# Kernel optimization log

Hardware: AMD Instinct MI355X
Metric: run time of the kernel (lower is better)

Reference implementation:

```python
import jax, jax.numpy as jnp
import numpy as np

B, L, DM, H = 2, 4096, 1024, 16
D = DM // H


def setup_inputs() -> dict:
    key = jax.random.key(0)
    ks = jax.random.split(key, 11)
    s = 1.0 / np.sqrt(DM)
    return {
        "query": jax.random.normal(ks[0], (B, L, DM), jnp.float32),
        "key": jax.random.normal(ks[1], (B, L, DM), jnp.float32),
        "value": jax.random.normal(ks[2], (B, L, DM), jnp.float32),
        "Wq": jax.random.normal(ks[3], (DM, DM), jnp.float32) * s,
        "bq": jnp.zeros((DM,), jnp.float32),
        "Wk": jax.random.normal(ks[4], (DM, DM), jnp.float32) * s,
        "bk": jnp.zeros((DM,), jnp.float32),
        "Wv": jax.random.normal(ks[5], (DM, DM), jnp.float32) * s,
        "bv": jnp.zeros((DM,), jnp.float32),
        "Wo": jax.random.normal(ks[6], (DM, DM), jnp.float32) * s,
        "bo": jnp.zeros((DM,), jnp.float32),
    }


def _split_heads(x):
    # (B, L, DM) -> (B, H, L, D)
    b, l, _ = x.shape
    return x.reshape(b, l, H, D).transpose(0, 2, 1, 3)


def reference(query, key, value, Wq, bq, Wk, bk, Wv, bv, Wo, bo):
    q = _split_heads(query @ Wq + bq)
    k = _split_heads(key @ Wk + bk)
    v = _split_heads(value @ Wv + bv)
    # ELU+1 feature map
    q = jax.nn.elu(q) + 1.0
    k = jax.nn.elu(k) + 1.0
    # Original: kv = einsum('bhld,bhmd->bhlm', k, v); out = einsum('bhlm,bhld->bhmd', kv, q)
    # Equivalent (associativity): out[m,d] = sum_e v[m,e] * (sum_l k[l,e] q[l,d])
    S = jnp.einsum('bhle,bhld->bhed', k, q)          # (B,H,D,D)
    out = jnp.einsum('bhme,bhed->bhmd', v, S)        # (B,H,L,D)
    denom = jnp.einsum('bhld,bhld->bhl', q, k) + 1e-6
    out = out / denom[..., None]
    # combine heads: (B,H,L,D) -> (B,L,DM)
    out = out.transpose(0, 2, 1, 3).reshape(out.shape[0], -1, DM)
    # out_dense; dropout is identity at inference
    return out @ Wo + bo
```

## Files before the change

### kernel.cpp

```cpp
#include <hip/hip_runtime.h>

#define B_  2
#define L_  4096
#define DM_ 1024
#define H_  16
#define D_  64
#define M_  (B_ * L_)

typedef unsigned short u16;
typedef short bf16x8 __attribute__((ext_vector_type(8)));
typedef float f32x4  __attribute__((ext_vector_type(4)));

typedef const __attribute__((address_space(1))) void* as1_cvp;
typedef __attribute__((address_space(3))) void* as3_vp;

__device__ __forceinline__ float b2f(u16 u) {
    union { unsigned int i; float f; } x; x.i = ((unsigned int)u) << 16; return x.f;
}
__device__ __forceinline__ u16 f2b(float f) {
    unsigned int x = __float_as_uint(f);
    return (u16)((x + 0x7fffu + ((x >> 16) & 1u)) >> 16);
}

__global__ void cast3_bf16_kernel(const float* __restrict__ i0, const float* __restrict__ i1,
                                  const float* __restrict__ i2,
                                  u16* __restrict__ o0, u16* __restrict__ o1, u16* __restrict__ o2,
                                  int n4) {
    int z = blockIdx.z;
    const float* in = z == 0 ? i0 : (z == 1 ? i1 : i2);
    u16* out       = z == 0 ? o0 : (z == 1 ? o1 : o2);
    int i = blockIdx.x * blockDim.x + threadIdx.x;
    if (i < n4) {
        float4 v = ((const float4*)in)[i];
        ushort4 o;
        o.x = f2b(v.x); o.y = f2b(v.y); o.z = f2b(v.z); o.w = f2b(v.w);
        ((ushort4*)out)[i] = o;
    }
}

__global__ void transpose4_cast_kernel(const float* __restrict__ w0, const float* __restrict__ w1,
                                       const float* __restrict__ w2, const float* __restrict__ w3,
                                       u16* __restrict__ t0, u16* __restrict__ t1,
                                       u16* __restrict__ t2, u16* __restrict__ t3) {
    int z = blockIdx.z;
    const float* W = z == 0 ? w0 : z == 1 ? w1 : z == 2 ? w2 : w3;
    u16* Wt        = z == 0 ? t0 : z == 1 ? t1 : z == 2 ? t2 : t3;
    __shared__ float tile[32][33];
    int tx = threadIdx.x, ty = threadIdx.y;
    int n = blockIdx.x * 32 + tx;
    int k0 = blockIdx.y * 32;
#pragma unroll
    for (int i = 0; i < 4; ++i)
        tile[ty + i * 8][tx] = W[(size_t)(k0 + ty + i * 8) * DM_ + n];
    __syncthreads();
#pragma unroll
    for (int i = 0; i < 4; ++i) {
        int nn = blockIdx.x * 32 + ty + i * 8;
        Wt[(size_t)nn * DM_ + k0 + tx] = f2b(tile[tx][ty + i * 8]);
    }
}

__global__ void zero_f32_kernel(float* __restrict__ p, int n) {
    int i = blockIdx.x * blockDim.x + threadIdx.x;
    if (i < n) p[i] = 0.f;
}

__global__ __launch_bounds__(256, 3) void gemm_qkv_kernel(
    const u16* __restrict__ qb, const u16* __restrict__ kb, const u16* __restrict__ vb,
    const u16* __restrict__ Wqt, const u16* __restrict__ Wkt, const u16* __restrict__ Wvt,
    const float* __restrict__ bq, const float* __restrict__ bk, const float* __restrict__ bv,
    u16* __restrict__ QpT, u16* __restrict__ KpT, u16* __restrict__ Vp)
{
    const int z = blockIdx.z;
    const u16* A    = z == 0 ? qb  : z == 1 ? kb  : vb;
    const u16* Bt   = z == 0 ? Wqt : z == 1 ? Wkt : Wvt;
    const float* bias = z == 0 ? bq : z == 1 ? bk : bv;

    __shared__ __align__(16) u16 smem[17408];
    u16* As = smem;
    u16* Bs = smem + 8192;

    const int t    = threadIdx.x;
    const int lane = t & 63;
    const int wave = t >> 6;
    const int wr   = wave >> 1;
    const int wc   = wave & 1;
    const int quad = lane >> 4;
    const int l16  = lane & 15;
    const int m0   = blockIdx.x * 128;
    const int n0   = blockIdx.y * 128;
    const int K    = DM_;

    f32x4 acc[4][4] = {};

    for (int kt = 0; kt < K; kt += 64) {
#pragma unroll
        for (int i = 0; i < 4; ++i) {
            int c   = i * 256 + t;
            int row = c >> 3;
            int kc  = c & 7;
            int cbase = i * 256 + wave * 64;
            const u16* gA = A  + (size_t)(m0 + row) * K + kt + kc * 8;
            const u16* gB = Bt + (size_t)(n0 + row) * K + kt + kc * 8;
            __builtin_amdgcn_global_load_lds((as1_cvp)gA, (as3_vp)(As + cbase * 8), 16, 0, 0);
            __builtin_amdgcn_global_load_lds((as1_cvp)gB, (as3_vp)(Bs + cbase * 8), 16, 0, 0);
        }
        __syncthreads();
#pragma unroll
        for (int ks = 0; ks < 2; ++ks) {
            bf16x8 af[4], bfr[4];
#pragma unroll
            for (int it = 0; it < 4; ++it)
                af[it] = *(const bf16x8*)(As + (wr * 64 + it * 16 + l16) * 64 + ks * 32 + quad * 8);
#pragma unroll
            for (int jt = 0; jt < 4; ++jt)
                bfr[jt] = *(const bf16x8*)(Bs + (wc * 64 + jt * 16 + l16) * 64 + ks * 32 + quad * 8);
#pragma unroll
            for (int it = 0; it < 4; ++it)
#pragma unroll
                for (int jt = 0; jt < 4; ++jt)
                    acc[it][jt] = __builtin_amdgcn_mfma_f32_16x16x32_bf16(
                        af[it], bfr[jt], acc[it][jt], 0, 0, 0);
        }
        __syncthreads();
    }

    if (z == 2) {
#pragma unroll
        for (int it = 0; it < 4; ++it) {
            int row0 = m0 + wr * 64 + it * 16 + quad * 4;
#pragma unroll
            for (int jt = 0; jt < 4; ++jt) {
                int col = n0 + wc * 64 + jt * 16 + l16;
                float bv2 = bias[col];
#pragma unroll
                for (int r = 0; r < 4; ++r)
                    Vp[(size_t)(row0 + r) * DM_ + col] = f2b(acc[it][jt][r] + bv2);
            }
        }
    } else {
        u16* OutT = z == 0 ? QpT : KpT;
        u16* Ct = smem;
#pragma unroll
        for (int it = 0; it < 4; ++it) {
            int row0 = wr * 64 + it * 16 + quad * 4;
#pragma unroll
            for (int jt = 0; jt < 4; ++jt) {
                int colr = wc * 64 + jt * 16 + l16;
                float bv2 = bias[n0 + colr];
                float x0 = acc[it][jt][0] + bv2;
                float x1 = acc[it][jt][1] + bv2;
                float x2 = acc[it][jt][2] + bv2;
                float x3 = acc[it][jt][3] + bv2;
                x0 = (x0 > 0.f) ? (x0 + 1.f) : __expf(x0);
                x1 = (x1 > 0.f) ? (x1 + 1.f) : __expf(x1);
                x2 = (x2 > 0.f) ? (x2 + 1.f) : __expf(x2);
                x3 = (x3 > 0.f) ? (x3 + 1.f) : __expf(x3);
                ushort4 o;
                o.x = f2b(x0); o.y = f2b(x1); o.z = f2b(x2); o.w = f2b(x3);
                *(ushort4*)&Ct[colr * 136 + row0] = o;
            }
        }
        __syncthreads();
        int b   = m0 >> 12;
        int seg = t & 15;
        int cg  = t >> 4;
#pragma unroll
        for (int iter = 0; iter < 8; ++iter) {
            int colIdx = iter * 16 + cg;
            int gcol = n0 + colIdx;
            int bh = b * 16 + (gcol >> 6);
            int e  = gcol & 63;
            uint4 v = *(const uint4*)&Ct[colIdx * 136 + seg * 8];
            *(uint4*)(OutT + ((size_t)bh << 18) + ((size_t)e << 12)
                      + (m0 & 4095) + seg * 8) = v;
        }
    }
}

__global__ __launch_bounds__(256, 3) void gemm_out_kernel(
    const u16* __restrict__ A, const u16* __restrict__ Bt,
    const float* __restrict__ bias, float* __restrict__ Cout)
{
    __shared__ __align__(16) u16 smem[16384];
    u16* As = smem;
    u16* Bs = smem + 8192;

    const int t    = threadIdx.x;
    const int lane = t & 63;
    const int wave = t >> 6;
    const int wr   = wave >> 1;
    const int wc   = wave & 1;
    const int quad = lane >> 4;
    const int l16  = lane & 15;
    const int m0   = blockIdx.x * 128;
    const int n0   = blockIdx.y * 128;
    const int K    = DM_;

    f32x4 acc[4][4] = {};

    for (int kt = 0; kt < K; kt += 64) {
#pragma unroll
        for (int i = 0; i < 4; ++i) {
            int c   = i * 256 + t;
            int row = c >> 3;
            int kc  = c & 7;
            int cbase = i * 256 + wave * 64;
            const u16* gA = A  + (size_t)(m0 + row) * K + kt + kc * 8;
            const u16* gB = Bt + (size_t)(n0 + row) * K + kt + kc * 8;
            __builtin_amdgcn_global_load_lds((as1_cvp)gA, (as3_vp)(As + cbase * 8), 16, 0, 0);
            __builtin_amdgcn_global_load_lds((as1_cvp)gB, (as3_vp)(Bs + cbase * 8), 16, 0, 0);
        }
        __syncthreads();
#pragma unroll
        for (int ks = 0; ks < 2; ++ks) {
            bf16x8 af[4], bfr[4];
#pragma unroll
            for (int it = 0; it < 4; ++it)
                af[it] = *(const bf16x8*)(As + (wr * 64 + it * 16 + l16) * 64 + ks * 32 + quad * 8);
#pragma unroll
            for (int jt = 0; jt < 4; ++jt)
                bfr[jt] = *(const bf16x8*)(Bs + (wc * 64 + jt * 16 + l16) * 64 + ks * 32 + quad * 8);
#pragma unroll
            for (int it = 0; it < 4; ++it)
#pragma unroll
                for (int jt = 0; jt < 4; ++jt)
                    acc[it][jt] = __builtin_amdgcn_mfma_f32_16x16x32_bf16(
                        af[it], bfr[jt], acc[it][jt], 0, 0, 0);
        }
        __syncthreads();
    }

#pragma unroll
    for (int it = 0; it < 4; ++it) {
        int row0 = m0 + wr * 64 + it * 16 + quad * 4;
#pragma unroll
        for (int jt = 0; jt < 4; ++jt) {
            int col = n0 + wc * 64 + jt * 16 + l16;
            float bv = bias[col];
#pragma unroll
            for (int r = 0; r < 4; ++r)
                Cout[(size_t)(row0 + r) * DM_ + col] = acc[it][jt][r] + bv;
        }
    }
}

__global__ __launch_bounds__(256) void attn_s_kernel(
    const u16* __restrict__ QpT, const u16* __restrict__ KpT,
    float* __restrict__ S, float* __restrict__ denom)
{
    const int t    = threadIdx.x;
    const int lane = t & 63;
    const int wave = t >> 6;
    const int quad = lane >> 4;
    const int l16  = lane & 15;
    const int bh   = blockIdx.x;
    const int lc   = blockIdx.y * 512;

    const u16* baseQ = QpT + ((size_t)bh << 18);
    const u16* baseK = KpT + ((size_t)bh << 18);

    f32x4 acc[4] = {};
    const u16* arow = baseK + (size_t)(wave * 16 + l16) * 4096 + lc;
#pragma unroll 4
    for (int ks = 0; ks < 16; ++ks) {
        int koff = ks * 32 + quad * 8;
        bf16x8 a = *(const bf16x8*)(arow + koff);
#pragma unroll
        for (int dt = 0; dt < 4; ++dt) {
            bf16x8 b = *(const bf16x8*)(baseQ + (size_t)(dt * 16 + l16) * 4096 + lc + koff);
            acc[dt] = __builtin_amdgcn_mfma_f32_16x16x32_bf16(a, b, acc[dt], 0, 0, 0);
        }
    }
    float* Sb = S + (size_t)bh * 4096;
#pragma unroll
    for (int dt = 0; dt < 4; ++dt)
#pragma unroll
        for (int r = 0; r < 4; ++r)
            atomicAdd(&Sb[(wave * 16 + quad * 4 + r) * 64 + dt * 16 + l16], acc[dt][r]);

    {
        float s0 = 0.f, s1 = 0.f;
        int off = lc + 2 * t;
#pragma unroll 8
        for (int e = 0; e < 64; ++e) {
            unsigned int qv = *(const unsigned int*)(baseQ + (size_t)e * 4096 + off);
            unsigned int kv = *(const unsigned int*)(baseK + (size_t)e * 4096 + off);
            s0 += b2f((u16)(qv & 0xffff)) * b2f((u16)(kv & 0xffff));
            s1 += b2f((u16)(qv >> 16))   * b2f((u16)(kv >> 16));
        }
        denom[(size_t)bh * 4096 + off]     = s0 + 1e-6f;
        denom[(size_t)bh * 4096 + off + 1] = s1 + 1e-6f;
    }
}

__global__ __launch_bounds__(256) void attn_out_kernel(
    const u16* __restrict__ Vp, const float* __restrict__ S,
    const float* __restrict__ denom, u16* __restrict__ ctx)
{
    __shared__ __align__(16) u16 Sb[64 * 64];
    __shared__ float dsh[256];
    const int t    = threadIdx.x;
    const int lane = t & 63;
    const int wave = t >> 6;
    const int quad = lane >> 4;
    const int l16  = lane & 15;
    const int bh   = blockIdx.x;
    const int b    = bh >> 4, h = bh & 15;
    const int lc   = blockIdx.y * 256;

    {
        const float* Sg = S + (size_t)bh * 4096;
        int e = t >> 2, d0 = (t & 3) * 16;
#pragma unroll
        for (int i = 0; i < 16; ++i)
            Sb[(d0 + i) * 64 + e] = f2b(Sg[e * 64 + d0 + i]);
        dsh[t] = denom[(size_t)bh * 4096 + lc + t];
    }
    __syncthreads();

    const u16* Abase = Vp + (size_t)b * L_ * DM_ + (size_t)(lc + wave * 64 + l16) * DM_ + h * 64;
    f32x4 acc[4][4] = {};
#pragma unroll
    for (int ks = 0; ks < 2; ++ks) {
        int koff = ks * 32 + quad * 8;
        bf16x8 af[4], bfr[4];
#pragma unroll
        for (int lt = 0; lt < 4; ++lt)
            af[lt] = *(const bf16x8*)(Abase + (size_t)(lt * 16) * DM_ + koff);
#pragma unroll
        for (int dt = 0; dt < 4; ++dt)
            bfr[dt] = *(const bf16x8*)(Sb + (dt * 16 + l16) * 64 + koff);
#pragma unroll
        for (int lt = 0; lt < 4; ++lt)
#pragma unroll
            for (int dt = 0; dt < 4; ++dt)
                acc[lt][dt] = __builtin_amdgcn_mfma_f32_16x16x32_bf16(
                    af[lt], bfr[dt], acc[lt][dt], 0, 0, 0);
    }

    u16* cbase = ctx + (size_t)b * L_ * DM_ + h * 64;
#pragma unroll
    for (int lt = 0; lt < 4; ++lt) {
        int lrow0 = wave * 64 + lt * 16 + quad * 4;
        float inv[4];
#pragma unroll
        for (int r = 0; r < 4; ++r) inv[r] = 1.f / dsh[lrow0 + r];
#pragma unroll
        for (int dt = 0; dt < 4; ++dt) {
            int d = dt * 16 + l16;
#pragma unroll
            for (int r = 0; r < 4; ++r)
                cbase[(size_t)(lc + lrow0 + r) * DM_ + d] = f2b(acc[lt][dt][r] * inv[r]);
        }
    }
}

extern "C" void kernel_launch(void* const* d_in, const int* in_sizes, int n_in,
                              void* d_out, int out_size, void* d_ws, size_t ws_size,
                              hipStream_t stream)
{
    const float* query = (const float*)d_in[0];
    const float* key   = (const float*)d_in[1];
    const float* value = (const float*)d_in[2];
    const float* Wq = (const float*)d_in[3];  const float* bq = (const float*)d_in[4];
    const float* Wk = (const float*)d_in[5];  const float* bk = (const float*)d_in[6];
    const float* Wv = (const float*)d_in[7];  const float* bv = (const float*)d_in[8];
    const float* Wo = (const float*)d_in[9];  const float* bo = (const float*)d_in[10];

    const size_t SZ = (size_t)M_ * DM_ * sizeof(u16);
    char* ws = (char*)d_ws;
    u16* qb  = (u16*)(ws + 0 * SZ);
    u16* kb  = (u16*)(ws + 1 * SZ);
    u16* vb  = (u16*)(ws + 2 * SZ);
    u16* QpT = (u16*)(ws + 3 * SZ);
    u16* KpT = (u16*)(ws + 4 * SZ);
    u16* Vp  = qb;
    u16* ctx = kb;
    u16* Wqt = (u16*)(ws + 5 * SZ);
    u16* Wkt = Wqt + (size_t)DM_ * DM_;
    u16* Wvt = Wkt + (size_t)DM_ * DM_;
    u16* Wot = Wvt + (size_t)DM_ * DM_;
    float* S     = (float*)(ws + 5 * SZ + 4 * (size_t)DM_ * DM_ * sizeof(u16));
    float* denom = S + (size_t)B_ * H_ * D_ * D_;
    u16* Vp2  = (u16*)((char*)(denom + (size_t)B_ * H_ * L_) + 256);
    u16* ctx2 = (u16*)((char*)Vp2 + SZ);
    Vp = Vp2; ctx = ctx2;

    transpose4_cast_kernel<<<dim3(32, 32, 4), dim3(32, 8), 0, stream>>>(
        Wq, Wk, Wv, Wo, Wqt, Wkt, Wvt, Wot);

    int n4 = M_ * DM_ / 4;
    cast3_bf16_kernel<<<dim3(n4 / 256, 1, 3), 256, 0, stream>>>(
        query, key, value, qb, kb, vb, n4);

    int nS = B_ * H_ * D_ * D_;
    zero_f32_kernel<<<nS / 256, 256, 0, stream>>>(S, nS);

    gemm_qkv_kernel<<<dim3(M_ / 128, DM_ / 128, 3), 256, 0, stream>>>(
        qb, kb, vb, Wqt, Wkt, Wvt, bq, bk, bv, QpT, KpT, Vp);

    attn_s_kernel<<<dim3(B_ * H_, L_ / 512), 256, 0, stream>>>(QpT, KpT, S, denom);

    attn_out_kernel<<<dim3(B_ * H_, L_ / 256), 256, 0, stream>>>(Vp, S, denom, ctx);

    gemm_out_kernel<<<dim3(M_ / 128, DM_ / 128), 256, 0, stream>>>(
        ctx, Wot, bo, (float*)d_out);
}
```

Before: 285.6 us.

## Merge prep kernels, replace S atomics with partials, shrink output GEMM tile

Merges the weight transpose-cast, the input cast and the zeroing of S into one prep kernel, which cuts launches. Replaces the atomicAdd accumulation of S with per-block partial sums that attn_out_kernel reduces over 8 slices. Shrinks LDS in the QKV GEMM, removing the transpose padding (stride 136 to 128), so it can raise launch bounds to 4 blocks per CU. Halves the output GEMM M tile to 64 rows to get more blocks and higher occupancy. Trade-offs: more LDS bank conflicts in the transpose staging, redundant partial-sum reads in every attn_out block, and lower per-block reuse in the output GEMM.

```diff
diff --git a/kernel.cpp b/kernel.cpp
--- a/kernel.cpp
+++ b/kernel.cpp
@@ -22,50 +22,48 @@
     return (u16)((x + 0x7fffu + ((x >> 16) & 1u)) >> 16);
 }
 
-__global__ void cast3_bf16_kernel(const float* __restrict__ i0, const float* __restrict__ i1,
-                                  const float* __restrict__ i2,
-                                  u16* __restrict__ o0, u16* __restrict__ o1, u16* __restrict__ o2,
-                                  int n4) {
-    int z = blockIdx.z;
-    const float* in = z == 0 ? i0 : (z == 1 ? i1 : i2);
-    u16* out       = z == 0 ? o0 : (z == 1 ? o1 : o2);
-    int i = blockIdx.x * blockDim.x + threadIdx.x;
-    if (i < n4) {
+__global__ void prep_kernel(
+    const float* __restrict__ query, const float* __restrict__ key, const float* __restrict__ value,
+    u16* __restrict__ qb, u16* __restrict__ kb, u16* __restrict__ vb,
+    const float* __restrict__ w0, const float* __restrict__ w1,
+    const float* __restrict__ w2, const float* __restrict__ w3,
+    u16* __restrict__ t0, u16* __restrict__ t1, u16* __restrict__ t2, u16* __restrict__ t3)
+{
+    __shared__ float tile[32][33];
+    const int bx = blockIdx.x;
+    const int t  = threadIdx.x;
+    if (bx < 24576) {
+        int z = bx >> 13;
+        int i = (bx & 8191) * 256 + t;
+        const float* in = z == 0 ? query : (z == 1 ? key : value);
+        u16* out        = z == 0 ? qb    : (z == 1 ? kb  : vb);
         float4 v = ((const float4*)in)[i];
         ushort4 o;
         o.x = f2b(v.x); o.y = f2b(v.y); o.z = f2b(v.z); o.w = f2b(v.w);
         ((ushort4*)out)[i] = o;
-    }
-}
-
-__global__ void transpose4_cast_kernel(const float* __restrict__ w0, const float* __restrict__ w1,
-                                       const float* __restrict__ w2, const float* __restrict__ w3,
-                                       u16* __restrict__ t0, u16* __restrict__ t1,
-                                       u16* __restrict__ t2, u16* __restrict__ t3) {
-    int z = blockIdx.z;
-    const float* W = z == 0 ? w0 : z == 1 ? w1 : z == 2 ? w2 : w3;
-    u16* Wt        = z == 0 ? t0 : z == 1 ? t1 : z == 2 ? t2 : t3;
-    __shared__ float tile[32][33];
-    int tx = threadIdx.x, ty = threadIdx.y;
-    int n = blockIdx.x * 32 + tx;
-    int k0 = blockIdx.y * 32;
-#pragma unroll
-    for (int i = 0; i < 4; ++i)
-        tile[ty + i * 8][tx] = W[(size_t)(k0 + ty + i * 8) * DM_ + n];
-    __syncthreads();
-#pragma unroll
-    for (int i = 0; i < 4; ++i) {
-        int nn = blockIdx.x * 32 + ty + i * 8;
-        Wt[(size_t)nn * DM_ + k0 + tx] = f2b(tile[tx][ty + i * 8]);
-    }
-}
-
-__global__ void zero_f32_kernel(float* __restrict__ p, int n) {
-    int i = blockIdx.x * blockDim.x + threadIdx.x;
-    if (i < n) p[i] = 0.f;
-}
-
-__global__ __launch_bounds__(256, 3) void gemm_qkv_kernel(
+    } else {
+        int bz = bx - 24576;
+        int z  = bz >> 10;
+        int rem = bz & 1023;
+        int gx = rem & 31, gy = rem >> 5;
+        const float* W = z == 0 ? w0 : z == 1 ? w1 : z == 2 ? w2 : w3;
+        u16* Wt        = z == 0 ? t0 : z == 1 ? t1 : z == 2 ? t2 : t3;
+        int tx = t & 31, ty = t >> 5;
+        int n  = gx * 32 + tx;
+        int k0 = gy * 32;
+#pragma unroll
+        for (int i = 0; i < 4; ++i)
+            tile[ty + i * 8][tx] = W[(size_t)(k0 + ty + i * 8) * DM_ + n];
+        __syncthreads();
+#pragma unroll
+        for (int i = 0; i < 4; ++i) {
+            int nn = gx * 32 + ty + i * 8;
+            Wt[(size_t)nn * DM_ + k0 + tx] = f2b(tile[tx][ty + i * 8]);
+        }
+    }
+}
+
+__global__ __launch_bounds__(256, 4) void gemm_qkv_kernel(
     const u16* __restrict__ qb, const u16* __restrict__ kb, const u16* __restrict__ vb,
     const u16* __restrict__ Wqt, const u16* __restrict__ Wkt, const u16* __restrict__ Wvt,
     const float* __restrict__ bq, const float* __restrict__ bk, const float* __restrict__ bv,
@@ -76,7 +74,7 @@
     const u16* Bt   = z == 0 ? Wqt : z == 1 ? Wkt : Wvt;
     const float* bias = z == 0 ? bq : z == 1 ? bk : bv;
 
-    __shared__ __align__(16) u16 smem[17408];
+    __shared__ __align__(16) u16 smem[16384];
     u16* As = smem;
     u16* Bs = smem + 8192;
 
@@ -141,6 +139,7 @@
     } else {
         u16* OutT = z == 0 ? QpT : KpT;
         u16* Ct = smem;
+        __syncthreads();
 #pragma unroll
         for (int it = 0; it < 4; ++it) {
             int row0 = wr * 64 + it * 16 + quad * 4;
@@ -158,7 +157,7 @@
                 x3 = (x3 > 0.f) ? (x3 + 1.f) : __expf(x3);
                 ushort4 o;
                 o.x = f2b(x0); o.y = f2b(x1); o.z = f2b(x2); o.w = f2b(x3);
-                *(ushort4*)&Ct[colr * 136 + row0] = o;
+                *(ushort4*)&Ct[colr * 128 + row0] = o;
             }
         }
         __syncthreads();
@@ -171,20 +170,20 @@
             int gcol = n0 + colIdx;
             int bh = b * 16 + (gcol >> 6);
             int e  = gcol & 63;
-            uint4 v = *(const uint4*)&Ct[colIdx * 136 + seg * 8];
+            uint4 v = *(const uint4*)&Ct[colIdx * 128 + seg * 8];
             *(uint4*)(OutT + ((size_t)bh << 18) + ((size_t)e << 12)
                       + (m0 & 4095) + seg * 8) = v;
         }
     }
 }
 
-__global__ __launch_bounds__(256, 3) void gemm_out_kernel(
+__global__ __launch_bounds__(256, 5) void gemm_out_kernel(
     const u16* __restrict__ A, const u16* __restrict__ Bt,
     const float* __restrict__ bias, float* __restrict__ Cout)
 {
-    __shared__ __align__(16) u16 smem[16384];
+    __shared__ __align__(16) u16 smem[12288];
     u16* As = smem;
-    u16* Bs = smem + 8192;
+    u16* Bs = smem + 4096;
 
     const int t    = threadIdx.x;
     const int lane = t & 63;
@@ -193,36 +192,43 @@
     const int wc   = wave & 1;
     const int quad = lane >> 4;
     const int l16  = lane & 15;
-    const int m0   = blockIdx.x * 128;
+    const int m0   = blockIdx.x * 64;
     const int n0   = blockIdx.y * 128;
     const int K    = DM_;
 
-    f32x4 acc[4][4] = {};
+    f32x4 acc[2][4] = {};
 
     for (int kt = 0; kt < K; kt += 64) {
+#pragma unroll
+        for (int i = 0; i < 2; ++i) {
+            int c   = i * 256 + t;
+            int row = c >> 3;
+            int kc  = c & 7;
+            int cbase = i * 256 + wave * 64;
+            const u16* gA = A + (size_t)(m0 + row) * K + kt + kc * 8;
+            __builtin_amdgcn_global_load_lds((as1_cvp)gA, (as3_vp)(As + cbase * 8), 16, 0, 0);
+        }
 #pragma unroll
         for (int i = 0; i < 4; ++i) {
             int c   = i * 256 + t;
             int row = c >> 3;
             int kc  = c & 7;
             int cbase = i * 256 + wave * 64;
-            const u16* gA = A  + (size_t)(m0 + row) * K + kt + kc * 8;
             const u16* gB = Bt + (size_t)(n0 + row) * K + kt + kc * 8;
-            __builtin_amdgcn_global_load_lds((as1_cvp)gA, (as3_vp)(As + cbase * 8), 16, 0, 0);
             __builtin_amdgcn_global_load_lds((as1_cvp)gB, (as3_vp)(Bs + cbase * 8), 16, 0, 0);
         }
         __syncthreads();
 #pragma unroll
         for (int ks = 0; ks < 2; ++ks) {
-            bf16x8 af[4], bfr[4];
-#pragma unroll
-            for (int it = 0; it < 4; ++it)
-                af[it] = *(const bf16x8*)(As + (wr * 64 + it * 16 + l16) * 64 + ks * 32 + quad * 8);
+            bf16x8 af[2], bfr[4];
+#pragma unroll
+            for (int it = 0; it < 2; ++it)
+                af[it] = *(const bf16x8*)(As + (wr * 32 + it * 16 + l16) * 64 + ks * 32 + quad * 8);
 #pragma unroll
             for (int jt = 0; jt < 4; ++jt)
                 bfr[jt] = *(const bf16x8*)(Bs + (wc * 64 + jt * 16 + l16) * 64 + ks * 32 + quad * 8);
 #pragma unroll
-            for (int it = 0; it < 4; ++it)
+            for (int it = 0; it < 2; ++it)
 #pragma unroll
                 for (int jt = 0; jt < 4; ++jt)
                     acc[it][jt] = __builtin_amdgcn_mfma_f32_16x16x32_bf16(
@@ -232,8 +238,8 @@
     }
 
 #pragma unroll
-    for (int it = 0; it < 4; ++it) {
-        int row0 = m0 + wr * 64 + it * 16 + quad * 4;
+    for (int it = 0; it < 2; ++it) {
+        int row0 = m0 + wr * 32 + it * 16 + quad * 4;
 #pragma unroll
         for (int jt = 0; jt < 4; ++jt) {
             int col = n0 + wc * 64 + jt * 16 + l16;
@@ -247,7 +253,7 @@
 
 __global__ __launch_bounds__(256) void attn_s_kernel(
     const u16* __restrict__ QpT, const u16* __restrict__ KpT,
-    float* __restrict__ S, float* __restrict__ denom)
+    float* __restrict__ S_part, float* __restrict__ denom)
 {
     const int t    = threadIdx.x;
     const int lane = t & 63;
@@ -272,12 +278,12 @@
             acc[dt] = __builtin_amdgcn_mfma_f32_16x16x32_bf16(a, b, acc[dt], 0, 0, 0);
         }
     }
-    float* Sb = S + (size_t)bh * 4096;
+    float* Sp = S_part + ((size_t)blockIdx.y * 32 + bh) * 4096;
 #pragma unroll
     for (int dt = 0; dt < 4; ++dt)
 #pragma unroll
         for (int r = 0; r < 4; ++r)
-            atomicAdd(&Sb[(wave * 16 + quad * 4 + r) * 64 + dt * 16 + l16], acc[dt][r]);
+            Sp[(wave * 16 + quad * 4 + r) * 64 + dt * 16 + l16] = acc[dt][r];
 
     {
         float s0 = 0.f, s1 = 0.f;
@@ -295,7 +301,7 @@
 }
 
 __global__ __launch_bounds__(256) void attn_out_kernel(
-    const u16* __restrict__ Vp, const float* __restrict__ S,
+    const u16* __restrict__ Vp, const float* __restrict__ S_part,
     const float* __restrict__ denom, u16* __restrict__ ctx)
 {
     __shared__ __align__(16) u16 Sb[64 * 64];
@@ -310,11 +316,20 @@
     const int lc   = blockIdx.y * 256;
 
     {
-        const float* Sg = S + (size_t)bh * 4096;
+        const float* Sg = S_part + (size_t)bh * 4096;
         int e = t >> 2, d0 = (t & 3) * 16;
+        float tmp[16];
+#pragma unroll
+        for (int i = 0; i < 16; ++i) tmp[i] = 0.f;
+#pragma unroll
+        for (int p = 0; p < 8; ++p) {
+            const float* Sgp = Sg + (size_t)p * 32 * 4096;
+#pragma unroll
+            for (int i = 0; i < 16; ++i) tmp[i] += Sgp[e * 64 + d0 + i];
+        }
 #pragma unroll
         for (int i = 0; i < 16; ++i)
-            Sb[(d0 + i) * 64 + e] = f2b(Sg[e * 64 + d0 + i]);
+            Sb[(d0 + i) * 64 + e] = f2b(tmp[i]);
         dsh[t] = denom[(size_t)bh * 4096 + lc + t];
     }
     __syncthreads();
@@ -375,35 +390,25 @@
     u16* vb  = (u16*)(ws + 2 * SZ);
     u16* QpT = (u16*)(ws + 3 * SZ);
     u16* KpT = (u16*)(ws + 4 * SZ);
-    u16* Vp  = qb;
-    u16* ctx = kb;
-    u16* Wqt = (u16*)(ws + 5 * SZ);
+    u16* Vp  = (u16*)(ws + 5 * SZ);
+    u16* ctx = (u16*)(ws + 6 * SZ);
+    u16* Wqt = (u16*)(ws + 7 * SZ);
     u16* Wkt = Wqt + (size_t)DM_ * DM_;
     u16* Wvt = Wkt + (size_t)DM_ * DM_;
     u16* Wot = Wvt + (size_t)DM_ * DM_;
-    float* S     = (float*)(ws + 5 * SZ + 4 * (size_t)DM_ * DM_ * sizeof(u16));
-    float* denom = S + (size_t)B_ * H_ * D_ * D_;
-    u16* Vp2  = (u16*)((char*)(denom + (size_t)B_ * H_ * L_) + 256);
-    u16* ctx2 = (u16*)((char*)Vp2 + SZ);
-    Vp = Vp2; ctx = ctx2;
-
-    transpose4_cast_kernel<<<dim3(32, 32, 4), dim3(32, 8), 0, stream>>>(
-        Wq, Wk, Wv, Wo, Wqt, Wkt, Wvt, Wot);
-
-    int n4 = M_ * DM_ / 4;
-    cast3_bf16_kernel<<<dim3(n4 / 256, 1, 3), 256, 0, stream>>>(
-        query, key, value, qb, kb, vb, n4);
-
-    int nS = B_ * H_ * D_ * D_;
-    zero_f32_kernel<<<nS / 256, 256, 0, stream>>>(S, nS);
+    float* S_part = (float*)(ws + 7 * SZ + 4 * (size_t)DM_ * DM_ * sizeof(u16));
+    float* denom  = S_part + (size_t)8 * 32 * 4096;
+
+    prep_kernel<<<28672, 256, 0, stream>>>(
+        query, key, value, qb, kb, vb, Wq, Wk, Wv, Wo, Wqt, Wkt, Wvt, Wot);
 
     gemm_qkv_kernel<<<dim3(M_ / 128, DM_ / 128, 3), 256, 0, stream>>>(
         qb, kb, vb, Wqt, Wkt, Wvt, bq, bk, bv, QpT, KpT, Vp);
 
-    attn_s_kernel<<<dim3(B_ * H_, L_ / 512), 256, 0, stream>>>(QpT, KpT, S, denom);
-
-    attn_out_kernel<<<dim3(B_ * H_, L_ / 256), 256, 0, stream>>>(Vp, S, denom, ctx);
-
-    gemm_out_kernel<<<dim3(M_ / 128, DM_ / 128), 256, 0, stream>>>(
+    attn_s_kernel<<<dim3(B_ * H_, L_ / 512), 256, 0, stream>>>(QpT, KpT, S_part, denom);
+
+    attn_out_kernel<<<dim3(B_ * H_, L_ / 256), 256, 0, stream>>>(Vp, S_part, denom, ctx);
+
+    gemm_out_kernel<<<dim3(M_ / 64, DM_ / 128), 256, 0, stream>>>(
         ctx, Wot, bo, (float*)d_out);
 }
```

After: 287.7 us. Within noise of the previous version (+0.8%).
